# Kernel tuning notes

Measured on AMD Instinct MI355X. Metric: run time of the kernel, lower is better.

The kernel has to match this reference:

```python
import jax, jax.numpy as jnp
import numpy as np
from jax import lax

T, B, IN, H = 512, 64, 1024, 2048


def setup_inputs() -> dict:
    key = jax.random.key(0)
    k1, k2, k3, k4, k5, k6 = jax.random.split(key, 6)
    inputs = jax.random.normal(k1, (T, B, IN), dtype=jnp.float32) * 0.1
    hidden = jax.random.normal(k2, (1, B, H), dtype=jnp.float32) * 0.1
    # i2h params (default nn.Linear init ~ small); h2h initialised per irnn_initializer
    Wi = jax.random.normal(k3, (H, IN), dtype=jnp.float32) * 0.02
    bi = jax.random.normal(k4, (H,), dtype=jnp.float32) * 0.01
    Wh = jnp.eye(H, dtype=jnp.float32) + jax.random.normal(k5, (H, H), dtype=jnp.float32) * 0.005
    bh = jax.random.normal(k6, (H,), dtype=jnp.float32) * 0.01
    return {"inputs": inputs, "hidden": hidden, "Wi": Wi, "bi": bi, "Wh": Wh, "bh": bh}


def reference(inputs, hidden, Wi, bi, Wh, bh):
    h0 = hidden[0]  # [B, H]
    # Precompute the input projection for all timesteps in one big GEMM
    x_proj = jnp.einsum('tbi,hi->tbh', inputs, Wi) + bi  # [T, B, H]

    def step(h, xp):
        h = jax.nn.relu(h @ Wh.T + bh + xp)
        return h, h

    h_last, outputs = lax.scan(step, h0, x_proj)
    return outputs, h_last[None]  # ([T,B,H], [1,B,H])
```

## Files before the change

kernel.cpp:

```cpp
#include <hip/hip_runtime.h>

#define T_DIM 512
#define B_DIM 64
#define IN_DIM 1024
#define H_DIM 2048
#define BH (B_DIM * H_DIM)
#define KT 16
#define KC (H_DIM / KT)
#define JT 32

__global__ __launch_bounds__(256) void irnn_xproj(
    const float* __restrict__ A, const float* __restrict__ Wi,
    const float* __restrict__ bi, const float* __restrict__ bh,
    float* __restrict__ out)
{
  __shared__ float As[32][132];
  __shared__ float Bs[32][132];
  const int tid = threadIdx.x;
  const int tx = tid & 15;
  const int ty = tid >> 4;
  const size_t row0 = (size_t)blockIdx.x * 128;
  const int    col0 = blockIdx.y * 128;
  float acc[8][8] = {};

  for (int k0 = 0; k0 < IN_DIM; k0 += 32) {
    #pragma unroll
    for (int i = 0; i < 4; ++i) {
      int f = tid + 256 * i;
      int r = f >> 3, c = f & 7;
      const float4 v = *reinterpret_cast<const float4*>(
          A + (row0 + r) * IN_DIM + k0 + c * 4);
      As[c*4+0][r] = v.x; As[c*4+1][r] = v.y;
      As[c*4+2][r] = v.z; As[c*4+3][r] = v.w;
    }
    #pragma unroll
    for (int i = 0; i < 4; ++i) {
      int f = tid + 256 * i;
      int r = f >> 3, c = f & 7;
      const float4 v = *reinterpret_cast<const float4*>(
          Wi + (size_t)(col0 + r) * IN_DIM + k0 + c * 4);
      Bs[c*4+0][r] = v.x; Bs[c*4+1][r] = v.y;
      Bs[c*4+2][r] = v.z; Bs[c*4+3][r] = v.w;
    }
    __syncthreads();
    #pragma unroll
    for (int k = 0; k < 32; ++k) {
      float a[8], b[8];
      #pragma unroll
      for (int i = 0; i < 8; i += 4)
        *reinterpret_cast<float4*>(&a[i]) =
            *reinterpret_cast<const float4*>(&As[k][ty*8 + i]);
      #pragma unroll
      for (int j = 0; j < 8; j += 4)
        *reinterpret_cast<float4*>(&b[j]) =
            *reinterpret_cast<const float4*>(&Bs[k][tx*8 + j]);
      #pragma unroll
      for (int i = 0; i < 8; ++i)
        #pragma unroll
        for (int j = 0; j < 8; ++j)
          acc[i][j] = fmaf(a[i], b[j], acc[i][j]);
    }
    __syncthreads();
  }

  float bias[8];
  #pragma unroll
  for (int j = 0; j < 8; j += 4) {
    float4 v1 = *reinterpret_cast<const float4*>(bi + col0 + tx*8 + j);
    float4 v2 = *reinterpret_cast<const float4*>(bh + col0 + tx*8 + j);
    bias[j+0] = v1.x + v2.x; bias[j+1] = v1.y + v2.y;
    bias[j+2] = v1.z + v2.z; bias[j+3] = v1.w + v2.w;
  }
  #pragma unroll
  for (int i = 0; i < 8; ++i) {
    size_t o = (row0 + ty*8 + i) * H_DIM + col0 + tx*8;
    #pragma unroll
    for (int j = 0; j < 8; j += 4) {
      float4 v;
      v.x = acc[i][j+0] + bias[j+0];
      v.y = acc[i][j+1] + bias[j+1];
      v.z = acc[i][j+2] + bias[j+2];
      v.w = acc[i][j+3] + bias[j+3];
      *reinterpret_cast<float4*>(out + o + j) = v;
    }
  }
}

__global__ __launch_bounds__(256) void irnn_transpose(
    const float* __restrict__ Wh, float* __restrict__ WhT)
{
  __shared__ float tile[64][68];
  const int tid = threadIdx.x;
  const int j0 = blockIdx.x * 64;
  const int k0 = blockIdx.y * 64;
  #pragma unroll
  for (int i = 0; i < 4; ++i) {
    int f = tid + 256 * i;
    int r = f >> 4, cq = f & 15;
    float4 v = *reinterpret_cast<const float4*>(
        Wh + (size_t)(j0 + r) * H_DIM + k0 + cq * 4);
    *reinterpret_cast<float4*>(&tile[r][cq*4]) = v;
  }
  __syncthreads();
  #pragma unroll
  for (int i = 0; i < 4; ++i) {
    int f = tid + 256 * i;
    int r2 = f >> 4, c2 = f & 15;
    float4 v;
    v.x = tile[c2*4+0][r2];
    v.y = tile[c2*4+1][r2];
    v.z = tile[c2*4+2][r2];
    v.w = tile[c2*4+3][r2];
    *reinterpret_cast<float4*>(WhT + (size_t)(k0 + r2) * H_DIM + j0 + c2*4) = v;
  }
}

__global__ __launch_bounds__(256) void irnn_step_gemm(
    const float* __restrict__ h_prev,
    const float* __restrict__ WhT,
    float* __restrict__ P)
{
  const int tid = threadIdx.x;
  const int tn = tid & 15;
  const int tm = tid >> 4;
  const int jt = blockIdx.x;
  const int kt = blockIdx.y;
  const int kc = kt * KC;
  const float* hp = h_prev + (size_t)(tm * 4) * H_DIM + kc;
  const float* wp = WhT + (size_t)kc * H_DIM + jt * 64 + tn * 4;
  float4 acc[4] = {};

  #pragma unroll 4
  for (int kg = 0; kg < KC / 4; ++kg) {
    float4 hv[4], wv[4];
    #pragma unroll
    for (int u = 0; u < 4; ++u)
      hv[u] = *reinterpret_cast<const float4*>(hp + (size_t)u * H_DIM + kg * 4);
    #pragma unroll
    for (int kk = 0; kk < 4; ++kk)
      wv[kk] = *reinterpret_cast<const float4*>(wp + (size_t)(kg * 4 + kk) * H_DIM);
    #pragma unroll
    for (int u = 0; u < 4; ++u) {
      const float* hu = reinterpret_cast<const float*>(&hv[u]);
      #pragma unroll
      for (int kk = 0; kk < 4; ++kk) {
        const float hs = hu[kk];
        acc[u].x = fmaf(hs, wv[kk].x, acc[u].x);
        acc[u].y = fmaf(hs, wv[kk].y, acc[u].y);
        acc[u].z = fmaf(hs, wv[kk].z, acc[u].z);
        acc[u].w = fmaf(hs, wv[kk].w, acc[u].w);
      }
    }
  }

  float* pb = P + (size_t)kt * BH + (size_t)(tm * 4) * H_DIM + jt * 64 + tn * 4;
  #pragma unroll
  for (int u = 0; u < 4; ++u)
    *reinterpret_cast<float4*>(pb + (size_t)u * H_DIM) = acc[u];
}

__global__ __launch_bounds__(128) void irnn_reduce(
    const float4* __restrict__ P4,
    float4* __restrict__ xp_out,
    float4* __restrict__ h_last)
{
  const int o4 = blockIdx.x * 128 + threadIdx.x;
  float4 a = xp_out[o4];
  float sx = 0.f, sy = 0.f, sz = 0.f, sw = 0.f;
  #pragma unroll
  for (int kt = 0; kt < KT; ++kt) {
    const float4 p = P4[(size_t)kt * (BH / 4) + o4];
    sx += p.x; sy += p.y; sz += p.z; sw += p.w;
  }
  a.x = fmaxf(a.x + sx, 0.f);
  a.y = fmaxf(a.y + sy, 0.f);
  a.z = fmaxf(a.z + sz, 0.f);
  a.w = fmaxf(a.w + sw, 0.f);
  xp_out[o4] = a;
  if (h_last) h_last[o4] = a;
}

extern "C" void kernel_launch(void* const* d_in, const int* in_sizes, int n_in,
                              void* d_out, int out_size, void* d_ws, size_t ws_size,
                              hipStream_t stream) {
  const float* inputs = (const float*)d_in[0];
  const float* hidden = (const float*)d_in[1];
  const float* Wi     = (const float*)d_in[2];
  const float* bi     = (const float*)d_in[3];
  const float* Wh     = (const float*)d_in[4];
  const float* bh     = (const float*)d_in[5];
  float* out = (float*)d_out;

  float* scratch = (ws_size >= (size_t)24 * 1024 * 1024)
                       ? (float*)d_ws : (float*)d_in[0];
  float* P   = scratch;
  float* WhT = scratch + (size_t)2 * 1024 * 1024;

  irnn_xproj<<<dim3(256, 16), 256, 0, stream>>>(inputs, Wi, bi, bh, out);
  irnn_transpose<<<dim3(32, 32), 256, 0, stream>>>(Wh, WhT);

  for (int t = 0; t < T_DIM; ++t) {
    const float* hp = (t == 0) ? hidden : out + (size_t)(t - 1) * BH;
    irnn_step_gemm<<<dim3(JT, KT), 256, 0, stream>>>(hp, WhT, P);
    float4* hl = (t == T_DIM - 1)
                     ? (float4*)(out + (size_t)T_DIM * BH) : nullptr;
    irnn_reduce<<<dim3(256), 128, 0, stream>>>(
        (const float4*)P, (float4*)(out + (size_t)t * BH), hl);
  }
}
```

Before: 14.86 ms.

## Replace per-step launches with persistent kernel holding Wh in registers and grid barrier

The 1024 per-timestep launches of a split-K GEMM plus reduce are replaced by one persistent kernel of 256 blocks. Each block keeps its slice of Wh in registers for all timesteps, stages the needed hidden rows into LDS with direct global-to-LDS loads and an XOR swizzle, reduces its partial sums within the block, and applies bias, ReLU and the store. Timesteps are ordered by an atomic-counter grid barrier, which removes launch overhead, the partial-sum buffer traffic and the separate transpose. The cost is a large register footprint (128 floats of weights per thread) and the requirement that all 256 blocks be co-resident, or the spin barrier will deadlock.

```diff
diff --git a/kernel.cpp b/kernel.cpp
--- a/kernel.cpp
+++ b/kernel.cpp
@@ -5,9 +5,12 @@
 #define IN_DIM 1024
 #define H_DIM 2048
 #define BH (B_DIM * H_DIM)
-#define KT 16
-#define KC (H_DIM / KT)
-#define JT 32
+
+#define NBLK 256
+#define NTHR 512
+#define BT   16
+#define JTW  32
+#define LDS_BYTES (BT * H_DIM * 4)
 
 __global__ __launch_bounds__(256) void irnn_xproj(
     const float* __restrict__ A, const float* __restrict__ Wi,
@@ -86,98 +89,105 @@
   }
 }
 
-__global__ __launch_bounds__(256) void irnn_transpose(
-    const float* __restrict__ Wh, float* __restrict__ WhT)
+__global__ __launch_bounds__(NTHR, 2) void irnn_persist(
+    const float* __restrict__ hidden,
+    const float* __restrict__ Wh,
+    float* __restrict__ out,
+    unsigned* __restrict__ cnt)
 {
-  __shared__ float tile[64][68];
+  extern __shared__ float lds[];
   const int tid = threadIdx.x;
-  const int j0 = blockIdx.x * 64;
-  const int k0 = blockIdx.y * 64;
+  const int jp = tid & 15;
+  const int kr = tid >> 4;
+  const int wv = tid >> 6;
+  const int ln = tid & 63;
+  const int bid = blockIdx.x;
+  const int b0 = (bid & 3) * BT;
+  const int j0 = (bid >> 2) * JTW;
+  const int j_base = j0 + jp * 2;
+
+  float Wr[2][64];
   #pragma unroll
-  for (int i = 0; i < 4; ++i) {
-    int f = tid + 256 * i;
-    int r = f >> 4, cq = f & 15;
-    float4 v = *reinterpret_cast<const float4*>(
-        Wh + (size_t)(j0 + r) * H_DIM + k0 + cq * 4);
-    *reinterpret_cast<float4*>(&tile[r][cq*4]) = v;
-  }
-  __syncthreads();
-  #pragma unroll
-  for (int i = 0; i < 4; ++i) {
-    int f = tid + 256 * i;
-    int r2 = f >> 4, c2 = f & 15;
-    float4 v;
-    v.x = tile[c2*4+0][r2];
-    v.y = tile[c2*4+1][r2];
-    v.z = tile[c2*4+2][r2];
-    v.w = tile[c2*4+3][r2];
-    *reinterpret_cast<float4*>(WhT + (size_t)(k0 + r2) * H_DIM + j0 + c2*4) = v;
-  }
-}
-
-__global__ __launch_bounds__(256) void irnn_step_gemm(
-    const float* __restrict__ h_prev,
-    const float* __restrict__ WhT,
-    float* __restrict__ P)
-{
-  const int tid = threadIdx.x;
-  const int tn = tid & 15;
-  const int tm = tid >> 4;
-  const int jt = blockIdx.x;
-  const int kt = blockIdx.y;
-  const int kc = kt * KC;
-  const float* hp = h_prev + (size_t)(tm * 4) * H_DIM + kc;
-  const float* wp = WhT + (size_t)kc * H_DIM + jt * 64 + tn * 4;
-  float4 acc[4] = {};
-
-  #pragma unroll 4
-  for (int kg = 0; kg < KC / 4; ++kg) {
-    float4 hv[4], wv[4];
-    #pragma unroll
-    for (int u = 0; u < 4; ++u)
-      hv[u] = *reinterpret_cast<const float4*>(hp + (size_t)u * H_DIM + kg * 4);
-    #pragma unroll
-    for (int kk = 0; kk < 4; ++kk)
-      wv[kk] = *reinterpret_cast<const float4*>(wp + (size_t)(kg * 4 + kk) * H_DIM);
-    #pragma unroll
-    for (int u = 0; u < 4; ++u) {
-      const float* hu = reinterpret_cast<const float*>(&hv[u]);
-      #pragma unroll
-      for (int kk = 0; kk < 4; ++kk) {
-        const float hs = hu[kk];
-        acc[u].x = fmaf(hs, wv[kk].x, acc[u].x);
-        acc[u].y = fmaf(hs, wv[kk].y, acc[u].y);
-        acc[u].z = fmaf(hs, wv[kk].z, acc[u].z);
-        acc[u].w = fmaf(hs, wv[kk].w, acc[u].w);
+  for (int s = 0; s < 2; ++s) {
+    const float* wrow = Wh + (size_t)(j_base + s) * H_DIM + kr * 64;
+    #pragma unroll
+    for (int q = 0; q < 16; ++q) {
+      const float4 w4 = *reinterpret_cast<const float4*>(wrow + q * 4);
+      Wr[s][q*4+0] = w4.x; Wr[s][q*4+1] = w4.y;
+      Wr[s][q*4+2] = w4.z; Wr[s][q*4+3] = w4.w;
+    }
+  }
+
+  const int krx = (kr & 7) << 2;
+
+  for (int t = 0; t < T_DIM; ++t) {
+    const float* hsrc = (t == 0) ? hidden : out + (size_t)(t - 1) * BH;
+
+    #pragma unroll
+    for (int i = 0; i < 16; ++i) {
+      const int idx = wv * 16 + i;
+      const int b = idx >> 3, r = idx & 7;
+      const int base4 = r * 256 + 4 * ln;
+      const int ksrc = base4 ^ (((base4 >> 6) & 7) << 2);
+      const float* g = hsrc + (size_t)(b0 + b) * H_DIM + ksrc;
+      float* l = lds + b * H_DIM + r * 256;
+      __builtin_amdgcn_global_load_lds(
+          (const __attribute__((address_space(1))) void*)g,
+          (__attribute__((address_space(3))) void*)l, 16, 0, 0);
+    }
+    __syncthreads();
+
+    float acc[BT][2];
+    #pragma unroll
+    for (int b = 0; b < BT; ++b) {
+      const float* hb = lds + b * H_DIM + kr * 64;
+      float a0 = 0.f, a1 = 0.f;
+      #pragma unroll
+      for (int q = 0; q < 16; ++q) {
+        const float4 h4 =
+            *reinterpret_cast<const float4*>(hb + ((q * 4) ^ krx));
+        a0 = fmaf(h4.x, Wr[0][q*4+0], a0); a1 = fmaf(h4.x, Wr[1][q*4+0], a1);
+        a0 = fmaf(h4.y, Wr[0][q*4+1], a0); a1 = fmaf(h4.y, Wr[1][q*4+1], a1);
+        a0 = fmaf(h4.z, Wr[0][q*4+2], a0); a1 = fmaf(h4.z, Wr[1][q*4+2], a1);
+        a0 = fmaf(h4.w, Wr[0][q*4+3], a0); a1 = fmaf(h4.w, Wr[1][q*4+3], a1);
       }
-    }
-  }
-
-  float* pb = P + (size_t)kt * BH + (size_t)(tm * 4) * H_DIM + jt * 64 + tn * 4;
-  #pragma unroll
-  for (int u = 0; u < 4; ++u)
-    *reinterpret_cast<float4*>(pb + (size_t)u * H_DIM) = acc[u];
-}
-
-__global__ __launch_bounds__(128) void irnn_reduce(
-    const float4* __restrict__ P4,
-    float4* __restrict__ xp_out,
-    float4* __restrict__ h_last)
-{
-  const int o4 = blockIdx.x * 128 + threadIdx.x;
-  float4 a = xp_out[o4];
-  float sx = 0.f, sy = 0.f, sz = 0.f, sw = 0.f;
-  #pragma unroll
-  for (int kt = 0; kt < KT; ++kt) {
-    const float4 p = P4[(size_t)kt * (BH / 4) + o4];
-    sx += p.x; sy += p.y; sz += p.z; sw += p.w;
-  }
-  a.x = fmaxf(a.x + sx, 0.f);
-  a.y = fmaxf(a.y + sy, 0.f);
-  a.z = fmaxf(a.z + sz, 0.f);
-  a.w = fmaxf(a.w + sw, 0.f);
-  xp_out[o4] = a;
-  if (h_last) h_last[o4] = a;
+      acc[b][0] = a0; acc[b][1] = a1;
+    }
+
+    __syncthreads();
+    #pragma unroll
+    for (int b = 0; b < BT; ++b) {
+      lds[(b * 32 + jp * 2 + 0) * 33 + kr] = acc[b][0];
+      lds[(b * 32 + jp * 2 + 1) * 33 + kr] = acc[b][1];
+    }
+    __syncthreads();
+
+    float sum = 0.f;
+    #pragma unroll
+    for (int k2 = 0; k2 < 32; ++k2) sum += lds[tid * 33 + k2];
+
+    const int bo = tid >> 5, jr = tid & 31;
+    const size_t oaddr =
+        (size_t)t * BH + (size_t)(b0 + bo) * H_DIM + j0 + jr;
+    const float v = fmaxf(out[oaddr] + sum, 0.f);
+    out[oaddr] = v;
+    if (t == T_DIM - 1)
+      out[(size_t)T_DIM * BH + (size_t)(b0 + bo) * H_DIM + j0 + jr] = v;
+
+    if (t < T_DIM - 1) {
+      __threadfence();
+      __syncthreads();
+      if (tid == 0) {
+        __hip_atomic_fetch_add(cnt, 1u, __ATOMIC_RELEASE,
+                               __HIP_MEMORY_SCOPE_AGENT);
+        const unsigned target = (unsigned)(t + 1) * NBLK;
+        while (__hip_atomic_load(cnt, __ATOMIC_ACQUIRE,
+                                 __HIP_MEMORY_SCOPE_AGENT) < target)
+          __builtin_amdgcn_s_sleep(2);
+      }
+      __syncthreads();
+    }
+  }
 }
 
 extern "C" void kernel_launch(void* const* d_in, const int* in_sizes, int n_in,
@@ -191,20 +201,13 @@
   const float* bh     = (const float*)d_in[5];
   float* out = (float*)d_out;
 
-  float* scratch = (ws_size >= (size_t)24 * 1024 * 1024)
-                       ? (float*)d_ws : (float*)d_in[0];
-  float* P   = scratch;
-  float* WhT = scratch + (size_t)2 * 1024 * 1024;
+  unsigned* cnt = (ws_size >= 4) ? (unsigned*)d_ws : (unsigned*)d_in[0];
 
   irnn_xproj<<<dim3(256, 16), 256, 0, stream>>>(inputs, Wi, bi, bh, out);
-  irnn_transpose<<<dim3(32, 32), 256, 0, stream>>>(Wh, WhT);
-
-  for (int t = 0; t < T_DIM; ++t) {
-    const float* hp = (t == 0) ? hidden : out + (size_t)(t - 1) * BH;
-    irnn_step_gemm<<<dim3(JT, KT), 256, 0, stream>>>(hp, WhT, P);
-    float4* hl = (t == T_DIM - 1)
-                     ? (float4*)(out + (size_t)T_DIM * BH) : nullptr;
-    irnn_reduce<<<dim3(256), 128, 0, stream>>>(
-        (const float4*)P, (float4*)(out + (size_t)t * BH), hl);
-  }
+
+  hipMemsetAsync(cnt, 0, 64, stream);
+
+  hipFuncSetAttribute((const void*)irnn_persist,
+                      hipFuncAttributeMaxDynamicSharedMemorySize, LDS_BYTES);
+  irnn_persist<<<NBLK, NTHR, LDS_BYTES, stream>>>(hidden, Wh, out, cnt);
 }
```

Result: slower. 47.14 ms (+217.3%).
